# Performance work log

Hardware: AMD Instinct MI355X
Metric: run time of the kernel (lower is better)

## Reference

```python
import jax, jax.numpy as jnp
import numpy as np

S, B, D, H, DH = 1024, 4, 1024, 16, 64


def setup_inputs() -> dict:
    key = jax.random.key(0)
    ks = jax.random.split(key, 12)
    inp = {
        "query": jax.random.normal(ks[0], (S, B, D), dtype=jnp.float32),
        "key": jax.random.normal(ks[1], (S, B, D), dtype=jnp.float32),
        "value": jax.random.normal(ks[2], (S, B, D), dtype=jnp.float32),
        "key_mask": jax.random.randint(ks[3], (S, B), 0, 2, dtype=jnp.int32),
        # per-head stacked projection weights (original loops nn.Linear per head)
        "Wq": jax.random.normal(ks[4], (H, D, DH), dtype=jnp.float32) * 0.02,
        "bq": jnp.zeros((H, DH), dtype=jnp.float32),
        "Wk": jax.random.normal(ks[5], (H, D, DH), dtype=jnp.float32) * 0.02,
        "bk": jnp.zeros((H, DH), dtype=jnp.float32),
        "Wv": jax.random.normal(ks[6], (H, D, DH), dtype=jnp.float32) * 0.02,
        "bv": jnp.zeros((H, DH), dtype=jnp.float32),
        "Wo": jax.random.normal(ks[7], (H * DH, D), dtype=jnp.float32) * 0.02,
        "bo": jnp.zeros((D,), dtype=jnp.float32),
    }
    return inp


def reference(query, key, value, key_mask, Wq, bq, Wk, bk, Wv, bv, Wo, bo):
    # query/key/value: [S, B, D] (seq-major, matching torch einsum 'imk,jmk->imj')
    q = jnp.einsum('smd,hdk->smhk', query, Wq) + bq  # [Sq, B, H, DH]
    k = jnp.einsum('smd,hdk->smhk', key, Wk) + bk    # [Sk, B, H, DH]
    v = jnp.einsum('smd,hdk->smhk', value, Wv) + bv  # [Sk, B, H, DH]

    scale = 1.0 / jnp.sqrt(jnp.float32(DH))
    scores = jnp.einsum('imhk,jmhk->himj', q, k) * scale  # [H, Sq, B, Sk]
    # key_mask: [Sk, B] -> transpose -> [B, Sk]; additive -1e18 masking
    scores = scores - key_mask.astype(jnp.float32).T * 1e18
    attn = jax.nn.softmax(scores, axis=-1)
    out = jnp.einsum('himj,jmhk->imhk', attn, v)  # [Sq, B, H, DH]
    concat = out.reshape(out.shape[0], out.shape[1], H * DH)
    return concat @ Wo + bo  # [Sq, B, D]
```

## Files before the change

### kernel.cpp

```cpp
#include <hip/hip_runtime.h>
#include <hip/hip_bf16.h>


typedef __attribute__((ext_vector_type(8))) short short8;
typedef __attribute__((ext_vector_type(4))) short short4_;
typedef __attribute__((ext_vector_type(4))) float f32x4;
typedef __attribute__((ext_vector_type(16))) float f32x16;
typedef __attribute__((ext_vector_type(8))) __bf16 bf16x8;
typedef __attribute__((ext_vector_type(4))) __bf16 bf16x4;

union B8 {
    short8 s;
    bf16x8 b;
    unsigned short u[8];
};
union B4 {
    short4_ s;
    bf16x4 b;
    unsigned short u[4];
    int i[2];
};

#if __has_builtin(__builtin_amdgcn_exp2f)
#define EXP2(x) __builtin_amdgcn_exp2f(x)
#else
#define EXP2(x) exp2f(x)
#endif
#if __has_builtin(__builtin_amdgcn_rcpf)
#define RCP(x) __builtin_amdgcn_rcpf(x)
#else
#define RCP(x) (1.0f / (x))
#endif

static __device__ __forceinline__ unsigned short f2bf_rne(float f) {
    union { float f; unsigned u; } v; v.f = f;
    unsigned r = v.u + 0x7FFFu + ((v.u >> 16) & 1u);
    return (unsigned short)(r >> 16);
}

static __device__ __forceinline__ void async_lds16(const void* g, const void* l) {
    __builtin_amdgcn_global_load_lds(
        (const __attribute__((address_space(1))) unsigned int*)(unsigned long long)g,
        (__attribute__((address_space(3))) unsigned int*)(unsigned int)(unsigned long long)l,
        16, 0, 0);
}

__global__ __launch_bounds__(256) void prep(
    const float* __restrict__ Wq, const float* __restrict__ Wk,
    const float* __restrict__ Wv, const float* __restrict__ Wo,
    const float* __restrict__ query, const float* __restrict__ key,
    const float* __restrict__ value,
    unsigned short* __restrict__ WT,
    unsigned short* __restrict__ qA, unsigned short* __restrict__ kA,
    unsigned short* __restrict__ vA) {
    const int t = threadIdx.x;
    const int z = blockIdx.z;

    if (z >= 4) {
        const int zz = z - 4;
        const int tensor = zz >> 2;
        const int part = zz & 3;
        const float* src = (tensor == 0) ? query : (tensor == 1) ? key : value;
        unsigned short* dst = (tensor == 0) ? qA : (tensor == 1) ? kA : vA;
        const int blk = blockIdx.y * 16 + blockIdx.x;
        const size_t base = (size_t)part * 1048576 + (size_t)blk * 4096 + t * 16;
        B8 w0, w1;
#pragma unroll
        for (int i = 0; i < 2; ++i) {
            f32x4 a = *(const f32x4*)(src + base + i * 8);
            f32x4 b = *(const f32x4*)(src + base + i * 8 + 4);
#pragma unroll
            for (int j = 0; j < 4; ++j) {
                (i ? w1 : w0).u[j] = f2bf_rne(a[j]);
                (i ? w1 : w0).u[4 + j] = f2bf_rne(b[j]);
            }
        }
        *(short8*)(dst + base) = w0.s;
        *(short8*)(dst + base + 8) = w1.s;
        return;
    }

    __shared__ float sT[64][65];
    const int dtile = blockIdx.x;
    const int sub = blockIdx.y;
    const float* src;
    int spitch;
    unsigned short* dst;
    if (z < 3) {
        const float* W = (z == 0) ? Wq : (z == 1) ? Wk : Wv;
        src = W + (size_t)sub * 65536 + (size_t)dtile * 64 * 64;
        spitch = 64;
        dst = WT + (size_t)z * 1048576 + (size_t)(sub * 64) * 1024 + dtile * 64;
    } else {
        src = Wo + (size_t)dtile * 64 * 1024 + sub * 64;
        spitch = 1024;
        dst = WT + (size_t)3 * 1048576 + (size_t)(sub * 64) * 1024 + dtile * 64;
    }

    const int r = t >> 2;
    const int cseg = (t & 3) * 16;
#pragma unroll
    for (int i = 0; i < 4; ++i) {
        f32x4 v = *(const f32x4*)(src + (size_t)r * spitch + cseg + i * 4);
#pragma unroll
        for (int j = 0; j < 4; ++j) sT[r][cseg + i * 4 + j] = v[j];
    }
    __syncthreads();
    B8 w0, w1;
#pragma unroll
    for (int i = 0; i < 8; ++i) {
        w0.u[i] = f2bf_rne(sT[cseg + i][r]);
        w1.u[i] = f2bf_rne(sT[cseg + 8 + i][r]);
    }
    *(short8*)(dst + (size_t)r * 1024 + cseg) = w0.s;
    *(short8*)(dst + (size_t)r * 1024 + cseg + 8) = w1.s;
}

template <bool OUT_F32, bool BIAS_ROW>
__device__ __forceinline__ void gemm128(unsigned short* __restrict__ sA,
                                        unsigned short* __restrict__ sB,
                                        const unsigned short* __restrict__ A,
                                        size_t lda,
                                        const unsigned short* __restrict__ Bt,
                                        size_t ldb,
                                        const float* __restrict__ bias,
                                        void* __restrict__ Cv, size_t ldc,
                                        float oscale, int row0, int col0) {
    const int t = threadIdx.x;
    const int w = t >> 6;
    const int lane = t & 63;
    const int quad = lane >> 4;
    const int l15 = lane & 15;
    const int wr = w >> 1;
    const int wc = w & 1;
    const int srow16 = lane >> 2;
    const int sgseg = (lane & 3) ^ ((lane >> 3) & 3);
    const int rseg = (quad ^ ((l15 >> 1) & 3)) * 8;

    f32x4 acc[4][4] = {};

    const unsigned short* agp = A + (size_t)(row0 + w * 32 + srow16) * lda + sgseg * 8;
    const unsigned short* agp2 = agp + (size_t)16 * lda;
    const unsigned short* bgp = Bt + (size_t)(col0 + w * 32 + srow16) * ldb + sgseg * 8;
    const unsigned short* bgp2 = bgp + (size_t)16 * ldb;
    const int ldsA0 = (w * 32) * 32;
    const int ldsA1 = (w * 32 + 16) * 32;

    auto STAGE = [&](int tt, int off) {
        const int k0 = tt * 32;
        async_lds16(agp + k0, sA + off + ldsA0);
        async_lds16(agp2 + k0, sA + off + ldsA1);
        async_lds16(bgp + k0, sB + off + ldsA0);
        async_lds16(bgp2 + k0, sB + off + ldsA1);
    };
    auto COMPUTE = [&](int off) {
        const unsigned short* sac = sA + off;
        const unsigned short* sbc = sB + off;
        B8 af[4], bf[4];
#pragma unroll
        for (int i = 0; i < 4; ++i)
            af[i].s = *(const short8*)&sac[(wr * 64 + i * 16 + l15) * 32 + rseg];
#pragma unroll
        for (int j = 0; j < 4; ++j)
            bf[j].s = *(const short8*)&sbc[(wc * 64 + j * 16 + l15) * 32 + rseg];
#pragma unroll
        for (int i = 0; i < 4; ++i)
#pragma unroll
            for (int j = 0; j < 4; ++j)
                acc[i][j] = __builtin_amdgcn_mfma_f32_16x16x32_bf16(af[i].b, bf[j].b,
                                                                    acc[i][j], 0, 0, 0);
    };

    STAGE(0, 0);
    STAGE(1, 4096);

    for (int t3 = 0; t3 < 30; t3 += 3) {
        asm volatile("s_waitcnt vmcnt(4)" ::: "memory");
        __builtin_amdgcn_s_barrier();
        STAGE(t3 + 2, 8192);
        COMPUTE(0);
        asm volatile("s_waitcnt vmcnt(4)" ::: "memory");
        __builtin_amdgcn_s_barrier();
        STAGE(t3 + 3, 0);
        COMPUTE(4096);
        asm volatile("s_waitcnt vmcnt(4)" ::: "memory");
        __builtin_amdgcn_s_barrier();
        STAGE(t3 + 4, 4096);
        COMPUTE(8192);
    }
    asm volatile("s_waitcnt vmcnt(4)" ::: "memory");
    __builtin_amdgcn_s_barrier();
    COMPUTE(0);
    asm volatile("s_waitcnt vmcnt(0)" ::: "memory");
    __builtin_amdgcn_s_barrier();
    COMPUTE(4096);

    float brow[4][4];
    if constexpr (BIAS_ROW) {
#pragma unroll
        for (int i = 0; i < 4; ++i)
#pragma unroll
            for (int r = 0; r < 4; ++r)
                brow[i][r] = bias[row0 + wr * 64 + i * 16 + quad * 4 + r];
    }
#pragma unroll
    for (int j = 0; j < 4; ++j) {
        const int col = col0 + wc * 64 + j * 16 + l15;
        const float bcol = BIAS_ROW ? 0.0f : bias[col];
#pragma unroll
        for (int i = 0; i < 4; ++i) {
#pragma unroll
            for (int r = 0; r < 4; ++r) {
                const int row = row0 + wr * 64 + i * 16 + quad * 4 + r;
                const size_t idx = (size_t)row * ldc + col;
                const float bb = BIAS_ROW ? brow[i][r] : bcol;
                const float val = (acc[i][j][r] + bb) * oscale;
                if constexpr (OUT_F32)
                    ((float*)Cv)[idx] = val;
                else
                    ((unsigned short*)Cv)[idx] = f2bf_rne(val);
            }
        }
    }
}

#define SCALE_L2E 0.18033688011112042f

__global__ __launch_bounds__(256) void qkv_gemm(
    const unsigned short* __restrict__ qA, const unsigned short* __restrict__ kA,
    const unsigned short* __restrict__ vA,
    const unsigned short* __restrict__ WT,
    const float* __restrict__ bq, const float* __restrict__ bk, const float* __restrict__ bv,
    unsigned short* q_o, unsigned short* k_o, unsigned short* vT_o) {
    __shared__ unsigned short sA[3 * 128 * 32];
    __shared__ unsigned short sB[3 * 128 * 32];
    const int p = blockIdx.z;
    if (p < 2) {
        const unsigned short* A = (p == 0) ? qA : kA;
        const unsigned short* Bt = WT + (size_t)p * 1048576;
        const float* bias = (p == 0) ? bq : bk;
        unsigned short* C = (p == 0) ? q_o : k_o;
        const float osc = (p == 0) ? SCALE_L2E : 1.0f;
        gemm128<false, false>(sA, sB, A, 1024, Bt, 1024, bias, C, 1024, osc,
                              blockIdx.x * 128, blockIdx.y * 128);
    } else {
        const int b = blockIdx.x >> 3;
        const int rt = blockIdx.x & 7;
        gemm128<false, true>(sA, sB, WT + (size_t)2 * 1048576, 1024,
                             vA + (size_t)b * 1024, 4096, bv,
                             vT_o + (size_t)b * 1048576, 1024, 1.0f,
                             rt * 128, blockIdx.y * 128);
    }
}

__global__ __launch_bounds__(256) void out_gemm(const unsigned short* __restrict__ A,
                                                const unsigned short* __restrict__ WT,
                                                const float* __restrict__ bo,
                                                float* __restrict__ C) {
    __shared__ unsigned short sA[3 * 128 * 32];
    __shared__ unsigned short sB[3 * 128 * 32];
    gemm128<true, false>(sA, sB, A, 1024, WT + (size_t)3 * 1048576, 1024, bo, C, 1024,
                         1.0f, blockIdx.x * 128, blockIdx.y * 128);
}

#define TP 72

#if __has_builtin(__builtin_amdgcn_mfma_f32_32x32x8bf16_1k)
#define HAVE_X8 1
#endif

__global__ __launch_bounds__(256) void attn_kernel(
    const unsigned short* __restrict__ q,
    const unsigned short* __restrict__ k,
    const unsigned short* __restrict__ vT,
    const int* __restrict__ key_mask,
    unsigned short* __restrict__ o) {
    __shared__ unsigned short sK[2][64 * TP];
    __shared__ unsigned short sVt[2][64 * TP];
    __shared__ float sBias[1024];
    __shared__ unsigned long long sBits[16];

    const int t = threadIdx.x;
    const int wave = t >> 6;
    const int lane = t & 63;
    const int n31 = lane & 31;
    const int hh = lane >> 5;

    const int L = blockIdx.x + 8 * (blockIdx.y + 4 * blockIdx.z);
    const int xcd = L & 7;
    const int kk = L >> 3;
    const int g = (xcd << 3) | (kk >> 3);
    const int qt = kk & 7;
    const int b = g & 3;
    const int h = g >> 2;
    const int q0w = qt * 128 + wave * 32;

    const int srow = t >> 3;
    const int sseg = t & 7;

#pragma unroll
    for (int i = 0; i < 4; ++i) {
        const int idx = i * 4 + wave;
        const int sk = idx * 64 + lane;
        unsigned long long bal = __ballot(key_mask[sk * 4 + b] != 0);
        if (lane == 0) sBits[idx] = bal;
    }
    __syncthreads();
#pragma unroll
    for (int i = 0; i < 4; ++i) {
        const int idx = t * 4 + i;
        const int r = idx & 15;
        const int hb = (idx >> 4) & 1;
        const int blk = (idx >> 5) & 1;
        const int kt = idx >> 6;
        const int row = (r & 3) + 8 * (r >> 2) + 4 * hb + blk * 32;
        sBias[idx] = ((sBits[kt] >> row) & 1ull) ? -16384.0f : 0.0f;
    }

    bf16x8 qf[4];
    {
        const unsigned short* qrow =
            q + ((size_t)(q0w + n31) * 4 + b) * 1024 + h * 64 + hh * 8;
#pragma unroll
        for (int kc = 0; kc < 4; ++kc) {
            B8 tmp;
            tmp.s = *(const short8*)(qrow + kc * 16);
            qf[kc] = tmp.b;
        }
    }

    f32x16 O0 = {}, O1 = {}, L_ = {};
    B4 ones;
#pragma unroll
    for (int j = 0; j < 4; ++j) ones.u[j] = 0x3F80;
#if !defined(HAVE_X8)
    B8 ones8;
#pragma unroll
    for (int j = 0; j < 8; ++j) ones8.u[j] = 0x3F80;
#endif

    const unsigned short* kbase = k + (size_t)b * 1024 + h * 64;
    const unsigned short* vtb = vT + ((size_t)(b * 16 + h) * 64) * 1024;

    {
        const unsigned short* kr = kbase + (size_t)srow * 4096 + sseg * 8;
        short8 ka = *(const short8*)kr;
        short8 kb2 = *(const short8*)(kr + (size_t)32 * 4096);
        const unsigned short* vr = vtb + (size_t)srow * 1024 + sseg * 8;
        short8 va = *(const short8*)vr;
        short8 vb2 = *(const short8*)(vr + (size_t)32 * 1024);
        *(short8*)&sK[0][srow * TP + sseg * 8] = ka;
        *(short8*)&sK[0][(32 + srow) * TP + sseg * 8] = kb2;
        *(short8*)&sVt[0][srow * TP + sseg * 8] = va;
        *(short8*)&sVt[0][(32 + srow) * TP + sseg * 8] = vb2;
    }

#pragma unroll 2
    for (int kt = 0; kt < 16; ++kt) {
        const int cur = kt & 1;
        __syncthreads();
        short8 nka, nkb, nva, nvb;
        if (kt < 15) {
            const int k0n = (kt + 1) * 64;
            const unsigned short* kr = kbase + (size_t)(k0n + srow) * 4096 + sseg * 8;
            nka = *(const short8*)kr;
            nkb = *(const short8*)(kr + (size_t)32 * 4096);
            const unsigned short* vr = vtb + (size_t)srow * 1024 + k0n + sseg * 8;
            nva = *(const short8*)vr;
            nvb = *(const short8*)(vr + (size_t)32 * 1024);
        }
        B4 pfr[2][4];
#pragma unroll
        for (int blk = 0; blk < 2; ++blk) {
            f32x16 c;
            const f32x4* bp = (const f32x4*)&sBias[((kt * 2 + blk) * 2 + hh) * 16];
#pragma unroll
            for (int i = 0; i < 4; ++i) {
                f32x4 x = bp[i];
#pragma unroll
                for (int j = 0; j < 4; ++j) c[i * 4 + j] = x[j];
            }
            __builtin_amdgcn_s_setprio(1);
#pragma unroll
            for (int kc = 0; kc < 4; ++kc) {
                B8 af;
                af.s = *(const short8*)&sK[cur][(blk * 32 + n31) * TP + kc * 16 + hh * 8];
                c = __builtin_amdgcn_mfma_f32_32x32x16_bf16(af.b, qf[kc], c, 0, 0, 0);
            }
            __builtin_amdgcn_s_setprio(0);
#pragma unroll
            for (int gg = 0; gg < 4; ++gg)
#pragma unroll
                for (int j = 0; j < 4; ++j)
                    pfr[blk][gg].b[j] = (__bf16)EXP2(c[gg * 4 + j]);
        }
#if defined(HAVE_X8)
        __builtin_amdgcn_s_setprio(1);
#pragma unroll
        for (int blk = 0; blk < 2; ++blk) {
#pragma unroll
            for (int gg = 0; gg < 4; ++gg) {
                const int sko = blk * 32 + gg * 8 + hh * 4;
                B4 b0, b1;
                b0.s = *(const short4_*)&sVt[cur][n31 * TP + sko];
                b1.s = *(const short4_*)&sVt[cur][(32 + n31) * TP + sko];
                O0 = __builtin_amdgcn_mfma_f32_32x32x8bf16_1k(pfr[blk][gg].s, b0.s, O0, 0, 0, 0);
                O1 = __builtin_amdgcn_mfma_f32_32x32x8bf16_1k(pfr[blk][gg].s, b1.s, O1, 0, 0, 0);
                L_ = __builtin_amdgcn_mfma_f32_32x32x8bf16_1k(pfr[blk][gg].s, ones.s, L_, 0, 0, 0);
            }
        }
        __builtin_amdgcn_s_setprio(0);
#else
        __builtin_amdgcn_s_setprio(1);
#pragma unroll
        for (int blk = 0; blk < 2; ++blk) {
            B4 par[4];
#pragma unroll
            for (int gg = 0; gg < 4; ++gg) {
                par[gg].i[0] = __shfl_xor(pfr[blk][gg].i[0], 32);
                par[gg].i[1] = __shfl_xor(pfr[blk][gg].i[1], 32);
            }
#pragma unroll
            for (int w = 0; w < 2; ++w) {
                const int gsel = 2 * w + hh;
                B4 lo = (hh == 0) ? pfr[blk][gsel] : par[gsel];
                B4 hi = (hh == 0) ? par[gsel] : pfr[blk][gsel];
                B8 afr;
#pragma unroll
                for (int j = 0; j < 4; ++j) {
                    afr.u[j] = lo.u[j];
                    afr.u[4 + j] = hi.u[j];
                }
                const int sko = blk * 32 + w * 16 + hh * 8;
                B8 b0, b1;
                b0.s = *(const short8*)&sVt[cur][n31 * TP + sko];
                b1.s = *(const short8*)&sVt[cur][(32 + n31) * TP + sko];
                O0 = __builtin_amdgcn_mfma_f32_32x32x16_bf16(afr.b, b0.b, O0, 0, 0, 0);
                O1 = __builtin_amdgcn_mfma_f32_32x32x16_bf16(afr.b, b1.b, O1, 0, 0, 0);
                L_ = __builtin_amdgcn_mfma_f32_32x32x16_bf16(afr.b, ones8.b, L_, 0, 0, 0);
            }
        }
        __builtin_amdgcn_s_setprio(0);
#endif
        if (kt < 15) {
            const int nb = 1 - cur;
            *(short8*)&sK[nb][srow * TP + sseg * 8] = nka;
            *(short8*)&sK[nb][(32 + srow) * TP + sseg * 8] = nkb;
            *(short8*)&sVt[nb][srow * TP + sseg * 8] = nva;
            *(short8*)&sVt[nb][(32 + srow) * TP + sseg * 8] = nvb;
        }
    }

    unsigned short* obase = o + ((size_t)q0w * 4 + b) * 1024 + h * 64 + n31;
#pragma unroll
    for (int r = 0; r < 16; ++r) {
        const int qr = (r & 3) + 8 * (r >> 2) + 4 * hh;
        const float inv = RCP(L_[r]);
        obase[(size_t)qr * 4096] = f2bf_rne(O0[r] * inv);
        obase[(size_t)qr * 4096 + 32] = f2bf_rne(O1[r] * inv);
    }
}

extern "C" void kernel_launch(void* const* d_in, const int* in_sizes, int n_in,
                              void* d_out, int out_size, void* d_ws, size_t ws_size,
                              hipStream_t stream) {
    const float* query = (const float*)d_in[0];
    const float* key_ = (const float*)d_in[1];
    const float* value = (const float*)d_in[2];
    const int* key_mask = (const int*)d_in[3];
    const float* Wq = (const float*)d_in[4];
    const float* bq = (const float*)d_in[5];
    const float* Wk = (const float*)d_in[6];
    const float* bk = (const float*)d_in[7];
    const float* Wv = (const float*)d_in[8];
    const float* bv = (const float*)d_in[9];
    const float* Wo = (const float*)d_in[10];
    const float* bo = (const float*)d_in[11];
    float* out = (float*)d_out;

    const size_t NE = (size_t)4096 * 1024;
    unsigned short* q_ws = (unsigned short*)d_ws;
    unsigned short* k_ws = q_ws + NE;
    unsigned short* v_ws = k_ws + NE;
    unsigned short* a_ws = v_ws + NE;
    unsigned short* wt_ws = a_ws + NE;

    unsigned short* qA = a_ws;
    unsigned short* kA = (unsigned short*)d_out;
    unsigned short* vA = kA + NE;

    prep<<<dim3(16, 16, 16), 256, 0, stream>>>(Wq, Wk, Wv, Wo, query, key_, value,
                                               wt_ws, qA, kA, vA);
    qkv_gemm<<<dim3(32, 8, 3), 256, 0, stream>>>(qA, kA, vA, wt_ws,
                                                 bq, bk, bv, q_ws, k_ws, v_ws);
    attn_kernel<<<dim3(8, 4, 16), 256, 0, stream>>>(q_ws, k_ws, v_ws, key_mask, a_ws);
    out_gemm<<<dim3(32, 8, 1), 256, 0, stream>>>(a_ws, wt_ws, bo, out);
}
```

Before: 199.9 us.

## Use async global-to-LDS triple-buffered K/V staging with XOR-swizzled layout

Replaces register-staged double-buffered K/V tile loads in the attention kernel with direct asynchronous global-to-LDS copies (async_lds16) into a three-stage ring buffer, synchronised with vmcnt waits and raw barriers. The padded row layout is replaced by an unpadded 64-wide layout with an XOR swizzle on 8-element column groups to avoid bank conflicts. This aims to hide global load latency better and free the registers that held prefetched tiles, at the cost of more LDS and reliance on vmcnt counting being exact.

Result: faster. 196.0 us, median of 2 (-2.0%).

```diff
diff --git a/kernel.cpp b/kernel.cpp
--- a/kernel.cpp
+++ b/kernel.cpp
@@ -263,8 +263,6 @@
                          1.0f, blockIdx.x * 128, blockIdx.y * 128);
 }
 
-#define TP 72
-
 #if __has_builtin(__builtin_amdgcn_mfma_f32_32x32x8bf16_1k)
 #define HAVE_X8 1
 #endif
@@ -275,8 +273,8 @@
     const unsigned short* __restrict__ vT,
     const int* __restrict__ key_mask,
     unsigned short* __restrict__ o) {
-    __shared__ unsigned short sK[2][64 * TP];
-    __shared__ unsigned short sVt[2][64 * TP];
+    __shared__ unsigned short sK[3 * 64 * 64];
+    __shared__ unsigned short sVt[3 * 64 * 64];
     __shared__ float sBias[1024];
     __shared__ unsigned long long sBits[16];
 
@@ -285,6 +283,7 @@
     const int lane = t & 63;
     const int n31 = lane & 31;
     const int hh = lane >> 5;
+    const int n7 = n31 & 7;
 
     const int L = blockIdx.x + 8 * (blockIdx.y + 4 * blockIdx.z);
     const int xcd = L & 7;
@@ -295,9 +294,6 @@
     const int h = g >> 2;
     const int q0w = qt * 128 + wave * 32;
 
-    const int srow = t >> 3;
-    const int sseg = t & 7;
-
 #pragma unroll
     for (int i = 0; i < 4; ++i) {
         const int idx = i * 4 + wave;
@@ -328,6 +324,7 @@
             qf[kc] = tmp.b;
         }
     }
+    __syncthreads();
 
     f32x16 O0 = {}, O1 = {}, L_ = {};
     B4 ones;
@@ -342,33 +339,32 @@
     const unsigned short* kbase = k + (size_t)b * 1024 + h * 64;
     const unsigned short* vtb = vT + ((size_t)(b * 16 + h) * 64) * 1024;
 
-    {
-        const unsigned short* kr = kbase + (size_t)srow * 4096 + sseg * 8;
-        short8 ka = *(const short8*)kr;
-        short8 kb2 = *(const short8*)(kr + (size_t)32 * 4096);
-        const unsigned short* vr = vtb + (size_t)srow * 1024 + sseg * 8;
-        short8 va = *(const short8*)vr;
-        short8 vb2 = *(const short8*)(vr + (size_t)32 * 1024);
-        *(short8*)&sK[0][srow * TP + sseg * 8] = ka;
-        *(short8*)&sK[0][(32 + srow) * TP + sseg * 8] = kb2;
-        *(short8*)&sVt[0][srow * TP + sseg * 8] = va;
-        *(short8*)&sVt[0][(32 + srow) * TP + sseg * 8] = vb2;
-    }
-
-#pragma unroll 2
-    for (int kt = 0; kt < 16; ++kt) {
-        const int cur = kt & 1;
-        __syncthreads();
-        short8 nka, nkb, nva, nvb;
-        if (kt < 15) {
-            const int k0n = (kt + 1) * 64;
-            const unsigned short* kr = kbase + (size_t)(k0n + srow) * 4096 + sseg * 8;
-            nka = *(const short8*)kr;
-            nkb = *(const short8*)(kr + (size_t)32 * 4096);
-            const unsigned short* vr = vtb + (size_t)srow * 1024 + k0n + sseg * 8;
-            nva = *(const short8*)vr;
-            nvb = *(const short8*)(vr + (size_t)32 * 1024);
-        }
+    const int lr8 = lane >> 3;
+    const int gc = (lane & 7) ^ lr8;
+    const unsigned short* kst0 = kbase + (size_t)(wave * 16 + lr8) * 4096 + gc * 8;
+    const unsigned short* kst1 = kst0 + (size_t)8 * 4096;
+    const unsigned short* vst0 = vtb + (size_t)(wave * 16 + lr8) * 1024 + gc * 8;
+    const unsigned short* vst1 = vst0 + (size_t)8 * 1024;
+    const int lds0 = (wave * 16) * 64;
+    const int lds1 = (wave * 16 + 8) * 64;
+
+    auto STAGE = [&](int tt, int boff) {
+        const size_t k0 = (size_t)tt * 64;
+        async_lds16(kst0 + k0 * 4096, sK + boff + lds0);
+        async_lds16(kst1 + k0 * 4096, sK + boff + lds1);
+        async_lds16(vst0 + k0, sVt + boff + lds0);
+        async_lds16(vst1 + k0, sVt + boff + lds1);
+    };
+
+    auto ITER = [&](int kt, int curB, int stT, int stB, bool doStage, bool last) {
+        if (last)
+            asm volatile("s_waitcnt vmcnt(0)" ::: "memory");
+        else
+            asm volatile("s_waitcnt vmcnt(4)" ::: "memory");
+        __builtin_amdgcn_s_barrier();
+        if (doStage) STAGE(stT, stB);
+        const unsigned short* sKc = sK + curB;
+        const unsigned short* sVc = sVt + curB;
         B4 pfr[2][4];
 #pragma unroll
         for (int blk = 0; blk < 2; ++blk) {
@@ -384,7 +380,8 @@
 #pragma unroll
             for (int kc = 0; kc < 4; ++kc) {
                 B8 af;
-                af.s = *(const short8*)&sK[cur][(blk * 32 + n31) * TP + kc * 16 + hh * 8];
+                af.s = *(const short8*)&sKc[(blk * 32 + n31) * 64 +
+                                            (((kc * 2 + hh) ^ n7) << 3)];
                 c = __builtin_amdgcn_mfma_f32_32x32x16_bf16(af.b, qf[kc], c, 0, 0, 0);
             }
             __builtin_amdgcn_s_setprio(0);
@@ -400,10 +397,10 @@
         for (int blk = 0; blk < 2; ++blk) {
 #pragma unroll
             for (int gg = 0; gg < 4; ++gg) {
-                const int sko = blk * 32 + gg * 8 + hh * 4;
+                const int sg = (((blk * 4 + gg) ^ n7) << 3) + hh * 4;
                 B4 b0, b1;
-                b0.s = *(const short4_*)&sVt[cur][n31 * TP + sko];
-                b1.s = *(const short4_*)&sVt[cur][(32 + n31) * TP + sko];
+                b0.s = *(const short4_*)&sVc[n31 * 64 + sg];
+                b1.s = *(const short4_*)&sVc[(32 + n31) * 64 + sg];
                 O0 = __builtin_amdgcn_mfma_f32_32x32x8bf16_1k(pfr[blk][gg].s, b0.s, O0, 0, 0, 0);
                 O1 = __builtin_amdgcn_mfma_f32_32x32x8bf16_1k(pfr[blk][gg].s, b1.s, O1, 0, 0, 0);
                 L_ = __builtin_amdgcn_mfma_f32_32x32x8bf16_1k(pfr[blk][gg].s, ones.s, L_, 0, 0, 0);
@@ -421,8 +418,8 @@
                 par[gg].i[1] = __shfl_xor(pfr[blk][gg].i[1], 32);
             }
 #pragma unroll
-            for (int w = 0; w < 2; ++w) {
-                const int gsel = 2 * w + hh;
+            for (int w2 = 0; w2 < 2; ++w2) {
+                const int gsel = 2 * w2 + hh;
                 B4 lo = (hh == 0) ? pfr[blk][gsel] : par[gsel];
                 B4 hi = (hh == 0) ? par[gsel] : pfr[blk][gsel];
                 B8 afr;
@@ -431,10 +428,11 @@
                     afr.u[j] = lo.u[j];
                     afr.u[4 + j] = hi.u[j];
                 }
-                const int sko = blk * 32 + w * 16 + hh * 8;
+                const int cg = blk * 4 + w2 * 2 + hh;
+                const int sg = (cg ^ n7) << 3;
                 B8 b0, b1;
-                b0.s = *(const short8*)&sVt[cur][n31 * TP + sko];
-                b1.s = *(const short8*)&sVt[cur][(32 + n31) * TP + sko];
+                b0.s = *(const short8*)&sVc[n31 * 64 + sg];
+                b1.s = *(const short8*)&sVc[(32 + n31) * 64 + sg];
                 O0 = __builtin_amdgcn_mfma_f32_32x32x16_bf16(afr.b, b0.b, O0, 0, 0, 0);
                 O1 = __builtin_amdgcn_mfma_f32_32x32x16_bf16(afr.b, b1.b, O1, 0, 0, 0);
                 L_ = __builtin_amdgcn_mfma_f32_32x32x16_bf16(afr.b, ones8.b, L_, 0, 0, 0);
@@ -442,14 +440,19 @@
         }
         __builtin_amdgcn_s_setprio(0);
 #endif
-        if (kt < 15) {
-            const int nb = 1 - cur;
-            *(short8*)&sK[nb][srow * TP + sseg * 8] = nka;
-            *(short8*)&sK[nb][(32 + srow) * TP + sseg * 8] = nkb;
-            *(short8*)&sVt[nb][srow * TP + sseg * 8] = nva;
-            *(short8*)&sVt[nb][(32 + srow) * TP + sseg * 8] = nvb;
-        }
-    }
+    };
+
+    STAGE(0, 0);
+    STAGE(1, 4096);
+    for (int t3 = 0; t3 < 12; t3 += 3) {
+        ITER(t3, 0, t3 + 2, 8192, true, false);
+        ITER(t3 + 1, 4096, t3 + 3, 0, true, false);
+        ITER(t3 + 2, 8192, t3 + 4, 4096, true, false);
+    }
+    ITER(12, 0, 14, 8192, true, false);
+    ITER(13, 4096, 15, 0, true, false);
+    ITER(14, 8192, 0, 0, false, false);
+    ITER(15, 0, 0, 0, false, true);
 
     unsigned short* obase = o + ((size_t)q0w * 4 + b) * 1024 + h * 64 + n31;
 #pragma unroll
```
